# Kernel optimization log

Measured on AMD Instinct MI355X. Metric: run time of the kernel, lower is better.

## Reference

```python
import jax, jax.numpy as jnp
import numpy as np

L, B, D = 1024, 128, 256  # max_seq_len, batch (dialogues), modality feature dim


def _lin_init(key, shape, fan_in):
    s = 1.0 / np.sqrt(fan_in)
    return jax.random.uniform(key, shape, jnp.float32, -s, s)


def setup_inputs() -> dict:
    key = jax.random.key(0)
    ks = jax.random.split(key, 12)
    inp = {
        'a': jax.random.normal(ks[0], (L, B, D), jnp.float32),
        'v': jax.random.normal(ks[1], (L, B, D), jnp.float32),
        'l': jax.random.normal(ks[2], (L, B, D), jnp.float32),
        # all dialogues padded to full length -> fixed node count (jit-friendly)
        'lengths': jnp.full((B,), L, dtype=jnp.int32),
        # modality transforms: Linear(mem_dim, cand_dim)
        'Wa': _lin_init(ks[3], (D, D), D), 'ba': jnp.zeros((D,), jnp.float32),
        'Wv': _lin_init(ks[4], (D, D), D), 'bv': jnp.zeros((D,), jnp.float32),
        'Wl': _lin_init(ks[5], (D, D), D), 'bl': jnp.zeros((D,), jnp.float32),
        # pairwise gates: Linear(3*mem_dim, 1)
        'Wav': _lin_init(ks[6], (1, 3 * D), 3 * D), 'bav': jnp.zeros((1,), jnp.float32),
        'Wal': _lin_init(ks[7], (1, 3 * D), 3 * D), 'bal': jnp.zeros((1,), jnp.float32),
        'Wvl': _lin_init(ks[8], (1, 3 * D), 3 * D), 'bvl': jnp.zeros((1,), jnp.float32),
    }
    return inp


def _graphify(x, lengths):
    # simple_batch_graphify: cat_j x[:lengths[j], j, :].  With lengths == L this is
    # exactly the batch-major flattening of the padded tensor (node order preserved).
    return jnp.transpose(x, (1, 0, 2)).reshape(-1, x.shape[-1])  # (B*L, D)


def reference(a, v, l, lengths, Wa, ba, Wv, bv, Wl, bl, Wav, bav, Wal, bal, Wvl, bvl):
    na = _graphify(a, lengths)  # (N, D)
    nv = _graphify(v, lengths)
    nl = _graphify(l, lengths)

    # MMGatedAttention, att_type='general', modals='avl' (dropout = eval identity)
    ha = jnp.tanh(na @ Wa.T + ba)
    hv = jnp.tanh(nv @ Wv.T + bv)
    hl = jnp.tanh(nl @ Wl.T + bl)

    z_av = jax.nn.sigmoid(jnp.concatenate([na, nv, na * nv], axis=-1) @ Wav.T + bav)  # (N,1)
    h_av = z_av * ha + (1.0 - z_av) * hv

    z_al = jax.nn.sigmoid(jnp.concatenate([na, nl, na * nl], axis=-1) @ Wal.T + bal)
    h_al = z_al * ha + (1.0 - z_al) * hl

    z_vl = jax.nn.sigmoid(jnp.concatenate([nv, nl, nv * nl], axis=-1) @ Wvl.T + bvl)
    h_vl = z_vl * hv + (1.0 - z_vl) * hl

    return jnp.concatenate([h_av, h_al, h_vl], axis=-1)  # (N, 3D)
```

## Files before the change

### kernel.cpp

```cpp
#include <hip/hip_runtime.h>
#include <hip/hip_bf16.h>

#define L_SEQ 1024
#define B_DLG 128
#define D_DIM 256
#define BM 32
#define THREADS 512
#define KSTEPS 8
#define NTILES (L_SEQ / BM)
#define NBLK (B_DLG * NTILES)
#define OBPAD 778

typedef __attribute__((ext_vector_type(8))) short short8;
typedef __attribute__((ext_vector_type(4))) float f32x4;

__device__ __forceinline__ unsigned short f_to_bfbits(float f) {
    unsigned int u = __float_as_uint(f);
    unsigned int r = (u + 0x7FFFu + ((u >> 16) & 1u)) >> 16;
    return (unsigned short)r;
}
__device__ __forceinline__ float fast_tanh(float x) {
    return 1.0f - 2.0f / (__expf(2.0f * x) + 1.0f);
}
__device__ __forceinline__ float fast_sigmoid(float x) {
    return 1.0f / (1.0f + __expf(-x));
}
__device__ __forceinline__ float dot4(float4 x, float4 w) {
    return x.x * w.x + x.y * w.y + x.z * w.z + x.w * w.w;
}

__global__ void wconv_kernel(const float* __restrict__ wa,
                             const float* __restrict__ wv,
                             const float* __restrict__ wl,
                             unsigned short* __restrict__ wb) {
    int i = blockIdx.x * blockDim.x + threadIdx.x;
    int mod  = i >> 13;
    int r    = i & 8191;
    int col  = r >> 5;
    int ks   = (r >> 2) & 7;
    int kblk = r & 3;
    const float* src = (mod == 0) ? wa : (mod == 1) ? wv : wl;
    const float4* s = (const float4*)(src + col * 256 + ks * 32 + kblk * 8);
    float4 lo = s[0], hi = s[1];
    short8 pk;
    pk[0] = (short)f_to_bfbits(lo.x); pk[1] = (short)f_to_bfbits(lo.y);
    pk[2] = (short)f_to_bfbits(lo.z); pk[3] = (short)f_to_bfbits(lo.w);
    pk[4] = (short)f_to_bfbits(hi.x); pk[5] = (short)f_to_bfbits(hi.y);
    pk[6] = (short)f_to_bfbits(hi.z); pk[7] = (short)f_to_bfbits(hi.w);
    int dst = mod * 8192 + (((col >> 4) * 8 + ks) << 6) + kblk * 16 + (col & 15);
    *(short8*)(wb + dst * 8) = pk;
}

__global__ __launch_bounds__(THREADS, 4)
void fused_kernel(const float* __restrict__ a,
                  const float* __restrict__ v,
                  const float* __restrict__ l,
                  const unsigned short* __restrict__ wbf,
                  const float* __restrict__ ba,
                  const float* __restrict__ bv,
                  const float* __restrict__ bl,
                  const float* __restrict__ wav, const float* __restrict__ bav,
                  const float* __restrict__ wal, const float* __restrict__ bal,
                  const float* __restrict__ wvl, const float* __restrict__ bvl,
                  float* __restrict__ out) {
    __shared__ __align__(16) char lds_raw[16 * OBPAD * 4];
    __shared__ float lds_z[3][BM];
#define LDS_A  ((unsigned short (*)[BM][D_DIM])lds_raw)
#define LDS_OB ((float (*)[OBPAD])lds_raw)

    const int tid  = threadIdx.x;
    const int wave = tid >> 6;
    const int lane = tid & 63;
    const int b    = blockIdx.x >> 5;
    const int t0   = (blockIdx.x & (NTILES - 1)) * BM;

    float4 fa[4], fv[4], fl[4];
#pragma unroll
    for (int i = 0; i < BM / 8; ++i) {
        const int row = wave + 8 * i;
        const size_t gbase = ((size_t)(t0 + row) * B_DLG + b) * D_DIM + lane * 4;
        fa[i] = *(const float4*)(a + gbase);
        fv[i] = *(const float4*)(v + gbase);
        fl[i] = *(const float4*)(l + gbase);
    }

    const int k0 = lane * 4;
    float4 gav0 = *(const float4*)(wav + k0);
    float4 gav1 = *(const float4*)(wav + 256 + k0);
    float4 gav2 = *(const float4*)(wav + 512 + k0);
    float4 gal0 = *(const float4*)(wal + k0);
    float4 gal1 = *(const float4*)(wal + 256 + k0);
    float4 gal2 = *(const float4*)(wal + 512 + k0);
    float4 gvl0 = *(const float4*)(wvl + k0);
    float4 gvl1 = *(const float4*)(wvl + 256 + k0);
    float4 gvl2 = *(const float4*)(wvl + 512 + k0);

    {
        const int swz = (wave & 7) << 4;
        const int boff = (lane * 8) ^ swz;
#pragma unroll
        for (int i = 0; i < BM / 8; ++i) {
            const int row = wave + 8 * i;
            ushort4 pa, pv, pl;
            pa.x = f_to_bfbits(fa[i].x); pa.y = f_to_bfbits(fa[i].y);
            pa.z = f_to_bfbits(fa[i].z); pa.w = f_to_bfbits(fa[i].w);
            pv.x = f_to_bfbits(fv[i].x); pv.y = f_to_bfbits(fv[i].y);
            pv.z = f_to_bfbits(fv[i].z); pv.w = f_to_bfbits(fv[i].w);
            pl.x = f_to_bfbits(fl[i].x); pl.y = f_to_bfbits(fl[i].y);
            pl.z = f_to_bfbits(fl[i].z); pl.w = f_to_bfbits(fl[i].w);
            *(ushort4*)((char*)&LDS_A[0][row][0] + boff) = pa;
            *(ushort4*)((char*)&LDS_A[1][row][0] + boff) = pv;
            *(ushort4*)((char*)&LDS_A[2][row][0] + boff) = pl;

            float4 pav, pal, pvl;
            pav.x = fa[i].x * fv[i].x; pav.y = fa[i].y * fv[i].y;
            pav.z = fa[i].z * fv[i].z; pav.w = fa[i].w * fv[i].w;
            pal.x = fa[i].x * fl[i].x; pal.y = fa[i].y * fl[i].y;
            pal.z = fa[i].z * fl[i].z; pal.w = fa[i].w * fl[i].w;
            pvl.x = fv[i].x * fl[i].x; pvl.y = fv[i].y * fl[i].y;
            pvl.z = fv[i].z * fl[i].z; pvl.w = fv[i].w * fl[i].w;
            float s_av = dot4(fa[i], gav0) + dot4(fv[i], gav1) + dot4(pav, gav2);
            float s_al = dot4(fa[i], gal0) + dot4(fl[i], gal1) + dot4(pal, gal2);
            float s_vl = dot4(fv[i], gvl0) + dot4(fl[i], gvl1) + dot4(pvl, gvl2);

#pragma unroll
            for (int off = 1; off < 64; off <<= 1) {
                s_av += __shfl_xor(s_av, off);
                s_al += __shfl_xor(s_al, off);
                s_vl += __shfl_xor(s_vl, off);
            }
            if (lane == 0) {
                lds_z[0][row] = fast_sigmoid(s_av + bav[0]);
                lds_z[1][row] = fast_sigmoid(s_al + bal[0]);
                lds_z[2][row] = fast_sigmoid(s_vl + bvl[0]);
            }
        }
    }
    __syncthreads();

    f32x4 acc[3][2][2];
#pragma unroll
    for (int m = 0; m < 3; ++m)
#pragma unroll
        for (int mt = 0; mt < 2; ++mt)
#pragma unroll
            for (int ct = 0; ct < 2; ++ct)
                acc[m][mt][ct] = (f32x4){0.f, 0.f, 0.f, 0.f};

    const int l15 = lane & 15;
    const int kblk = lane >> 4;
    const int colbase = wave * 32;

#pragma unroll 2
    for (int ks = 0; ks < KSTEPS; ++ks) {
        int kbyte = ks * 64 + kblk * 16;
#pragma unroll
        for (int mod = 0; mod < 3; ++mod) {
            short8 afrag[2];
#pragma unroll
            for (int mt = 0; mt < 2; ++mt) {
                int row = mt * 16 + l15;
                int bo = kbyte ^ ((row & 7) << 4);
                afrag[mt] = *(const short8*)((const char*)&LDS_A[mod][row][0] + bo);
            }
#pragma unroll
            for (int ct = 0; ct < 2; ++ct) {
                const unsigned short* bp = wbf +
                    ((size_t)(((mod * 16 + wave * 2 + ct) * 8 + ks) * 64) + lane) * 8;
                short8 bfrag = *(const short8*)bp;
#pragma unroll
                for (int mt = 0; mt < 2; ++mt)
                    acc[mod][mt][ct] = __builtin_amdgcn_mfma_f32_16x16x32_bf16(
                        afrag[mt], bfrag, acc[mod][mt][ct], 0, 0, 0);
            }
        }
    }

    const int col0 = colbase + l15, col1 = colbase + 16 + l15;
    const float bba0 = ba[col0], bba1 = ba[col1];
    const float bbv0 = bv[col0], bbv1 = bv[col1];
    const float bbl0 = bl[col0], bbl1 = bl[col1];

    const size_t rowbase = (size_t)b * L_SEQ + t0;
#pragma unroll
    for (int half = 0; half < 2; ++half) {
        __syncthreads();
        const int mt = half;
#pragma unroll
        for (int ct = 0; ct < 2; ++ct) {
            const int col = (ct == 0) ? col0 : col1;
            const float bba = (ct == 0) ? bba0 : bba1;
            const float bbv = (ct == 0) ? bbv0 : bbv1;
            const float bbl = (ct == 0) ? bbl0 : bbl1;
#pragma unroll
            for (int r = 0; r < 4; ++r) {
                const int rh = kblk * 4 + r;
                float ta = fast_tanh(acc[0][mt][ct][r] + bba);
                float tv = fast_tanh(acc[1][mt][ct][r] + bbv);
                float tl = fast_tanh(acc[2][mt][ct][r] + bbl);
                float zav = lds_z[0][mt * 16 + rh];
                float zal = lds_z[1][mt * 16 + rh];
                float zvl = lds_z[2][mt * 16 + rh];
                LDS_OB[rh][col]             = zav * ta + (1.f - zav) * tv;
                LDS_OB[rh][D_DIM + col]     = zal * ta + (1.f - zal) * tl;
                LDS_OB[rh][2 * D_DIM + col] = zvl * tv + (1.f - zvl) * tl;
            }
        }
        __syncthreads();
#pragma unroll
        for (int r2 = 0; r2 < 2; ++r2) {
            const int row = wave * 2 + r2;
#pragma unroll
            for (int s = 0; s < 3; ++s) {
                float4 val = *(const float4*)&LDS_OB[row][s * D_DIM + lane * 4];
                *(float4*)(out + (rowbase + half * 16 + row) * (3 * D_DIM)
                               + s * D_DIM + lane * 4) = val;
            }
        }
    }
#undef LDS_A
#undef LDS_OB
}

extern "C" void kernel_launch(void* const* d_in, const int* in_sizes, int n_in,
                              void* d_out, int out_size, void* d_ws, size_t ws_size,
                              hipStream_t stream) {
    const float* a   = (const float*)d_in[0];
    const float* v   = (const float*)d_in[1];
    const float* l   = (const float*)d_in[2];
    const float* Wa  = (const float*)d_in[4];
    const float* ba  = (const float*)d_in[5];
    const float* Wv  = (const float*)d_in[6];
    const float* bv  = (const float*)d_in[7];
    const float* Wl  = (const float*)d_in[8];
    const float* bl  = (const float*)d_in[9];
    const float* Wav = (const float*)d_in[10];
    const float* bav = (const float*)d_in[11];
    const float* Wal = (const float*)d_in[12];
    const float* bal = (const float*)d_in[13];
    const float* Wvl = (const float*)d_in[14];
    const float* bvl = (const float*)d_in[15];
    float* out = (float*)d_out;

    unsigned short* wb = (unsigned short*)d_ws;

    hipLaunchKernelGGL(wconv_kernel, dim3(96), dim3(256), 0, stream, Wa, Wv, Wl, wb);
    hipLaunchKernelGGL(fused_kernel, dim3(NBLK), dim3(THREADS), 0, stream,
                       a, v, l, wb, ba, bv, bl, Wav, bav, Wal, bal, Wvl, bvl, out);
}
```

Baseline: 247.3 us.

## Use per-wave LDS staging for output epilogue to drop block barriers

Replaces the block-wide two-half output staging, which needed __syncthreads between phases, with a per-wave private LDS tile (32x36 floats) that each wave writes and reads back under only a waitcnt. Tanh is now applied once to all accumulators up front, and the gate blend is rewritten as h2 + z*(h1-h2). Output stores become 128-byte row segments per wave instead of full 1 KB rows, which may lower global write coalescing, and the WAR safety against the last MFMA reads relies on the added lds_barrier.

```diff
diff --git a/kernel.cpp b/kernel.cpp
--- a/kernel.cpp
+++ b/kernel.cpp
@@ -9,7 +9,7 @@
 #define KSTEPS 8
 #define NTILES (L_SEQ / BM)
 #define NBLK (B_DLG * NTILES)
-#define OBPAD 778
+#define OBROW 36
 
 typedef __attribute__((ext_vector_type(8))) short short8;
 typedef __attribute__((ext_vector_type(4))) float f32x4;
@@ -27,6 +27,12 @@
 }
 __device__ __forceinline__ float dot4(float4 x, float4 w) {
     return x.x * w.x + x.y * w.y + x.z * w.z + x.w * w.w;
+}
+
+__device__ __forceinline__ void lds_barrier() {
+    asm volatile("s_waitcnt lgkmcnt(0)" ::: "memory");
+    __builtin_amdgcn_s_barrier();
+    __builtin_amdgcn_sched_barrier(0);
 }
 
 __global__ void wconv_kernel(const float* __restrict__ wa,
@@ -63,10 +69,9 @@
                   const float* __restrict__ wal, const float* __restrict__ bal,
                   const float* __restrict__ wvl, const float* __restrict__ bvl,
                   float* __restrict__ out) {
-    __shared__ __align__(16) char lds_raw[16 * OBPAD * 4];
+    __shared__ __align__(16) char lds_raw[3 * BM * D_DIM * 2];
     __shared__ float lds_z[3][BM];
-#define LDS_A  ((unsigned short (*)[BM][D_DIM])lds_raw)
-#define LDS_OB ((float (*)[OBPAD])lds_raw)
+#define LDS_A ((unsigned short (*)[BM][D_DIM])lds_raw)
 
     const int tid  = threadIdx.x;
     const int wave = tid >> 6;
@@ -136,7 +141,7 @@
             }
         }
     }
-    __syncthreads();
+    lds_barrier();
 
     f32x4 acc[3][2][2];
 #pragma unroll
@@ -176,50 +181,55 @@
         }
     }
 
+    lds_barrier();
+
     const int col0 = colbase + l15, col1 = colbase + 16 + l15;
     const float bba0 = ba[col0], bba1 = ba[col1];
     const float bbv0 = bv[col0], bbv1 = bv[col1];
     const float bbl0 = bl[col0], bbl1 = bl[col1];
 
+#pragma unroll
+    for (int mt = 0; mt < 2; ++mt)
+#pragma unroll
+        for (int ct = 0; ct < 2; ++ct)
+#pragma unroll
+            for (int r = 0; r < 4; ++r) {
+                acc[0][mt][ct][r] = fast_tanh(acc[0][mt][ct][r] + (ct ? bba1 : bba0));
+                acc[1][mt][ct][r] = fast_tanh(acc[1][mt][ct][r] + (ct ? bbv1 : bbv0));
+                acc[2][mt][ct][r] = fast_tanh(acc[2][mt][ct][r] + (ct ? bbl1 : bbl0));
+            }
+
+    float* ob = (float*)lds_raw + wave * (BM * OBROW);
     const size_t rowbase = (size_t)b * L_SEQ + t0;
-#pragma unroll
-    for (int half = 0; half < 2; ++half) {
-        __syncthreads();
-        const int mt = half;
-#pragma unroll
-        for (int ct = 0; ct < 2; ++ct) {
-            const int col = (ct == 0) ? col0 : col1;
-            const float bba = (ct == 0) ? bba0 : bba1;
-            const float bbv = (ct == 0) ? bbv0 : bbv1;
-            const float bbl = (ct == 0) ? bbl0 : bbl1;
-#pragma unroll
-            for (int r = 0; r < 4; ++r) {
-                const int rh = kblk * 4 + r;
-                float ta = fast_tanh(acc[0][mt][ct][r] + bba);
-                float tv = fast_tanh(acc[1][mt][ct][r] + bbv);
-                float tl = fast_tanh(acc[2][mt][ct][r] + bbl);
-                float zav = lds_z[0][mt * 16 + rh];
-                float zal = lds_z[1][mt * 16 + rh];
-                float zvl = lds_z[2][mt * 16 + rh];
-                LDS_OB[rh][col]             = zav * ta + (1.f - zav) * tv;
-                LDS_OB[rh][D_DIM + col]     = zal * ta + (1.f - zal) * tl;
-                LDS_OB[rh][2 * D_DIM + col] = zvl * tv + (1.f - zvl) * tl;
-            }
+
+#pragma unroll
+    for (int sec = 0; sec < 3; ++sec) {
+        const int mA = (sec == 2) ? 1 : 0;
+        const int mB = (sec == 0) ? 1 : 2;
+#pragma unroll
+        for (int mt = 0; mt < 2; ++mt)
+#pragma unroll
+            for (int ct = 0; ct < 2; ++ct)
+#pragma unroll
+                for (int r = 0; r < 4; ++r) {
+                    const int row = mt * 16 + kblk * 4 + r;
+                    const float h1 = acc[mA][mt][ct][r];
+                    const float h2 = acc[mB][mt][ct][r];
+                    const float z  = lds_z[sec][row];
+                    ob[row * OBROW + ct * 16 + l15] = h2 + z * (h1 - h2);
+                }
+        asm volatile("s_waitcnt lgkmcnt(0)" ::: "memory");
+        __builtin_amdgcn_sched_barrier(0);
+#pragma unroll
+        for (int q = 0; q < 4; ++q) {
+            const int rt   = q * 8 + (lane >> 3);
+            const int colq = lane & 7;
+            float4 val = *(const float4*)&ob[rt * OBROW + colq * 4];
+            *(float4*)(out + (rowbase + rt) * (3 * D_DIM)
+                           + sec * D_DIM + wave * 32 + colq * 4) = val;
         }
-        __syncthreads();
-#pragma unroll
-        for (int r2 = 0; r2 < 2; ++r2) {
-            const int row = wave * 2 + r2;
-#pragma unroll
-            for (int s = 0; s < 3; ++s) {
-                float4 val = *(const float4*)&LDS_OB[row][s * D_DIM + lane * 4];
-                *(float4*)(out + (rowbase + half * 16 + row) * (3 * D_DIM)
-                               + s * D_DIM + lane * 4) = val;
-            }
-        }
     }
 #undef LDS_A
-#undef LDS_OB
 }
 
 extern "C" void kernel_launch(void* const* d_in, const int* in_sizes, int n_in,
```

Result: slower. 255.4 us (+3.2%).

## Split fused kernel into pack and GEMM kernels via workspace fragments

Applied to the files above, without the earlier changes.

Splits the single fused kernel into two. A pack kernel converts a/v/l to bf16 MFMA-fragment layout and computes the sigmoid gates, writing both to workspace. A GEMM kernel then reads those fragments directly from global memory, applies tanh and the gating, and writes output through a per-wave LDS staging buffer. This separates the gate/conversion phase from the matrix-multiply phase and lowers LDS pressure in the GEMM. The cost is an extra round trip of bf16 fragments and gates through HBM, and an extra launch; the old fused kernel is kept as a fallback when the workspace is too small.

```diff
diff --git a/kernel.cpp b/kernel.cpp
--- a/kernel.cpp
+++ b/kernel.cpp
@@ -8,8 +8,16 @@
 #define THREADS 512
 #define KSTEPS 8
 #define NTILES (L_SEQ / BM)
-#define NBLK (B_DLG * NTILES)
+#define NTILE_TOT (B_DLG * NTILES)
+#define OBROW 36
 #define OBPAD 778
+
+#define WS_WB_BYTES   ((size_t)(3 * 65536 * 2))
+#define WS_AFRAG_OFF  WS_WB_BYTES
+#define WS_AFRAG_BYTES ((size_t)NTILE_TOT * 48 * 1024)
+#define WS_Z_OFF      (WS_AFRAG_OFF + WS_AFRAG_BYTES)
+#define WS_Z_BYTES    ((size_t)3 * L_SEQ * B_DLG * 4)
+#define WS_NEED       (WS_Z_OFF + WS_Z_BYTES)
 
 typedef __attribute__((ext_vector_type(8))) short short8;
 typedef __attribute__((ext_vector_type(4))) float f32x4;
@@ -52,21 +60,16 @@
 }
 
 __global__ __launch_bounds__(THREADS, 4)
-void fused_kernel(const float* __restrict__ a,
-                  const float* __restrict__ v,
-                  const float* __restrict__ l,
-                  const unsigned short* __restrict__ wbf,
-                  const float* __restrict__ ba,
-                  const float* __restrict__ bv,
-                  const float* __restrict__ bl,
-                  const float* __restrict__ wav, const float* __restrict__ bav,
-                  const float* __restrict__ wal, const float* __restrict__ bal,
-                  const float* __restrict__ wvl, const float* __restrict__ bvl,
-                  float* __restrict__ out) {
-    __shared__ __align__(16) char lds_raw[16 * OBPAD * 4];
+void pack_kernel(const float* __restrict__ a,
+                 const float* __restrict__ v,
+                 const float* __restrict__ l,
+                 const float* __restrict__ wav, const float* __restrict__ bav,
+                 const float* __restrict__ wal, const float* __restrict__ bal,
+                 const float* __restrict__ wvl, const float* __restrict__ bvl,
+                 unsigned short* __restrict__ afrag,
+                 float* __restrict__ zbuf) {
+    __shared__ __align__(16) unsigned short lds_a[3][BM][D_DIM];
     __shared__ float lds_z[3][BM];
-#define LDS_A  ((unsigned short (*)[BM][D_DIM])lds_raw)
-#define LDS_OB ((float (*)[OBPAD])lds_raw)
 
     const int tid  = threadIdx.x;
     const int wave = tid >> 6;
@@ -76,7 +79,7 @@
 
     float4 fa[4], fv[4], fl[4];
 #pragma unroll
-    for (int i = 0; i < BM / 8; ++i) {
+    for (int i = 0; i < 4; ++i) {
         const int row = wave + 8 * i;
         const size_t gbase = ((size_t)(t0 + row) * B_DLG + b) * D_DIM + lane * 4;
         fa[i] = *(const float4*)(a + gbase);
@@ -99,7 +102,218 @@
         const int swz = (wave & 7) << 4;
         const int boff = (lane * 8) ^ swz;
 #pragma unroll
-        for (int i = 0; i < BM / 8; ++i) {
+        for (int i = 0; i < 4; ++i) {
+            const int row = wave + 8 * i;
+            ushort4 pa, pv, pl;
+            pa.x = f_to_bfbits(fa[i].x); pa.y = f_to_bfbits(fa[i].y);
+            pa.z = f_to_bfbits(fa[i].z); pa.w = f_to_bfbits(fa[i].w);
+            pv.x = f_to_bfbits(fv[i].x); pv.y = f_to_bfbits(fv[i].y);
+            pv.z = f_to_bfbits(fv[i].z); pv.w = f_to_bfbits(fv[i].w);
+            pl.x = f_to_bfbits(fl[i].x); pl.y = f_to_bfbits(fl[i].y);
+            pl.z = f_to_bfbits(fl[i].z); pl.w = f_to_bfbits(fl[i].w);
+            *(ushort4*)((char*)&lds_a[0][row][0] + boff) = pa;
+            *(ushort4*)((char*)&lds_a[1][row][0] + boff) = pv;
+            *(ushort4*)((char*)&lds_a[2][row][0] + boff) = pl;
+
+            float4 pav, pal, pvl;
+            pav.x = fa[i].x * fv[i].x; pav.y = fa[i].y * fv[i].y;
+            pav.z = fa[i].z * fv[i].z; pav.w = fa[i].w * fv[i].w;
+            pal.x = fa[i].x * fl[i].x; pal.y = fa[i].y * fl[i].y;
+            pal.z = fa[i].z * fl[i].z; pal.w = fa[i].w * fl[i].w;
+            pvl.x = fv[i].x * fl[i].x; pvl.y = fv[i].y * fl[i].y;
+            pvl.z = fv[i].z * fl[i].z; pvl.w = fv[i].w * fl[i].w;
+            float s_av = dot4(fa[i], gav0) + dot4(fv[i], gav1) + dot4(pav, gav2);
+            float s_al = dot4(fa[i], gal0) + dot4(fl[i], gal1) + dot4(pal, gal2);
+            float s_vl = dot4(fv[i], gvl0) + dot4(fl[i], gvl1) + dot4(pvl, gvl2);
+#pragma unroll
+            for (int off = 1; off < 64; off <<= 1) {
+                s_av += __shfl_xor(s_av, off);
+                s_al += __shfl_xor(s_al, off);
+                s_vl += __shfl_xor(s_vl, off);
+            }
+            if (lane == 0) {
+                lds_z[0][row] = fast_sigmoid(s_av + bav[0]);
+                lds_z[1][row] = fast_sigmoid(s_al + bal[0]);
+                lds_z[2][row] = fast_sigmoid(s_vl + bvl[0]);
+            }
+        }
+    }
+    __syncthreads();
+
+    const int l15 = lane & 15;
+    const int kblk = lane >> 4;
+    const size_t tbase = (size_t)blockIdx.x * 48;
+#pragma unroll
+    for (int j = 0; j < 6; ++j) {
+        const int c   = wave * 6 + j;
+        const int mod = c >> 4;
+        const int rem = c & 15;
+        const int mt  = rem >> 3;
+        const int ks  = rem & 7;
+        const int row = mt * 16 + l15;
+        const int bo  = (ks * 64 + kblk * 16) ^ ((row & 7) << 4);
+        short8 frag = *(const short8*)((const char*)&lds_a[mod][row][0] + bo);
+        *(short8*)(afrag + (tbase + c) * 512 + lane * 8) = frag;
+    }
+    if (tid < 96) {
+        const int sec = tid >> 5, row = tid & 31;
+        zbuf[sec * (L_SEQ * B_DLG) + blockIdx.x * BM + row] = lds_z[sec][row];
+    }
+}
+
+__global__ __launch_bounds__(THREADS, 4)
+void gemm_kernel(const unsigned short* __restrict__ afrag,
+                 const unsigned short* __restrict__ wbf,
+                 const float* __restrict__ zbuf,
+                 const float* __restrict__ ba,
+                 const float* __restrict__ bv,
+                 const float* __restrict__ bl,
+                 float* __restrict__ out) {
+    __shared__ __align__(16) float lds_ob[8][BM * OBROW];
+
+    const int tid  = threadIdx.x;
+    const int wave = tid >> 6;
+    const int lane = tid & 63;
+    const int l15  = lane & 15;
+    const int kblk = lane >> 4;
+    const size_t tile = blockIdx.x;
+
+    f32x4 acc[3][2][2];
+#pragma unroll
+    for (int m = 0; m < 3; ++m)
+#pragma unroll
+        for (int mt = 0; mt < 2; ++mt)
+#pragma unroll
+            for (int ct = 0; ct < 2; ++ct)
+                acc[m][mt][ct] = (f32x4){0.f, 0.f, 0.f, 0.f};
+
+#pragma unroll 2
+    for (int ks = 0; ks < KSTEPS; ++ks) {
+#pragma unroll
+        for (int mod = 0; mod < 3; ++mod) {
+            short8 afr[2];
+#pragma unroll
+            for (int mt = 0; mt < 2; ++mt) {
+                const int c = (mod * 2 + mt) * 8 + ks;
+                afr[mt] = *(const short8*)(afrag + (tile * 48 + c) * 512 + lane * 8);
+            }
+#pragma unroll
+            for (int ct = 0; ct < 2; ++ct) {
+                const unsigned short* bp = wbf +
+                    ((size_t)(((mod * 16 + wave * 2 + ct) * 8 + ks) * 64) + lane) * 8;
+                short8 bfrag = *(const short8*)bp;
+#pragma unroll
+                for (int mt = 0; mt < 2; ++mt)
+                    acc[mod][mt][ct] = __builtin_amdgcn_mfma_f32_16x16x32_bf16(
+                        afr[mt], bfrag, acc[mod][mt][ct], 0, 0, 0);
+            }
+        }
+    }
+
+    float zr[3][2][4];
+#pragma unroll
+    for (int sec = 0; sec < 3; ++sec)
+#pragma unroll
+        for (int mt = 0; mt < 2; ++mt)
+#pragma unroll
+            for (int r = 0; r < 4; ++r)
+                zr[sec][mt][r] = zbuf[sec * (L_SEQ * B_DLG) + tile * BM
+                                      + mt * 16 + kblk * 4 + r];
+
+    const int colbase = wave * 32;
+    const int col0 = colbase + l15, col1 = colbase + 16 + l15;
+    const float bba0 = ba[col0], bba1 = ba[col1];
+    const float bbv0 = bv[col0], bbv1 = bv[col1];
+    const float bbl0 = bl[col0], bbl1 = bl[col1];
+#pragma unroll
+    for (int mt = 0; mt < 2; ++mt)
+#pragma unroll
+        for (int ct = 0; ct < 2; ++ct)
+#pragma unroll
+            for (int r = 0; r < 4; ++r) {
+                acc[0][mt][ct][r] = fast_tanh(acc[0][mt][ct][r] + (ct ? bba1 : bba0));
+                acc[1][mt][ct][r] = fast_tanh(acc[1][mt][ct][r] + (ct ? bbv1 : bbv0));
+                acc[2][mt][ct][r] = fast_tanh(acc[2][mt][ct][r] + (ct ? bbl1 : bbl0));
+            }
+
+    float* ob = lds_ob[wave];
+    const size_t rowbase = tile * BM;
+#pragma unroll
+    for (int sec = 0; sec < 3; ++sec) {
+        const int mA = (sec == 2) ? 1 : 0;
+        const int mB = (sec == 0) ? 1 : 2;
+#pragma unroll
+        for (int mt = 0; mt < 2; ++mt)
+#pragma unroll
+            for (int ct = 0; ct < 2; ++ct)
+#pragma unroll
+                for (int r = 0; r < 4; ++r) {
+                    const int row = mt * 16 + kblk * 4 + r;
+                    const float h1 = acc[mA][mt][ct][r];
+                    const float h2 = acc[mB][mt][ct][r];
+                    const float z  = zr[sec][mt][r];
+                    ob[row * OBROW + ct * 16 + l15] = h2 + z * (h1 - h2);
+                }
+        asm volatile("s_waitcnt lgkmcnt(0)" ::: "memory");
+        __builtin_amdgcn_sched_barrier(0);
+#pragma unroll
+        for (int q = 0; q < 4; ++q) {
+            const int rt   = q * 8 + (lane >> 3);
+            const int colq = lane & 7;
+            float4 val = *(const float4*)&ob[rt * OBROW + colq * 4];
+            *(float4*)(out + (rowbase + rt) * (3 * D_DIM)
+                           + sec * D_DIM + wave * 32 + colq * 4) = val;
+        }
+    }
+}
+
+__global__ __launch_bounds__(THREADS, 4)
+void fused_fallback(const float* __restrict__ a,
+                    const float* __restrict__ v,
+                    const float* __restrict__ l,
+                    const unsigned short* __restrict__ wbf,
+                    const float* __restrict__ ba,
+                    const float* __restrict__ bv,
+                    const float* __restrict__ bl,
+                    const float* __restrict__ wav, const float* __restrict__ bav,
+                    const float* __restrict__ wal, const float* __restrict__ bal,
+                    const float* __restrict__ wvl, const float* __restrict__ bvl,
+                    float* __restrict__ out) {
+    __shared__ __align__(16) char lds_raw[16 * OBPAD * 4];
+    __shared__ float lds_z[3][BM];
+#define LDS_A  ((unsigned short (*)[BM][D_DIM])lds_raw)
+#define LDS_OB ((float (*)[OBPAD])lds_raw)
+
+    const int tid  = threadIdx.x;
+    const int wave = tid >> 6;
+    const int lane = tid & 63;
+    const int b    = blockIdx.x >> 5;
+    const int t0   = (blockIdx.x & (NTILES - 1)) * BM;
+
+    float4 fa[4], fv[4], fl[4];
+#pragma unroll
+    for (int i = 0; i < 4; ++i) {
+        const int row = wave + 8 * i;
+        const size_t gbase = ((size_t)(t0 + row) * B_DLG + b) * D_DIM + lane * 4;
+        fa[i] = *(const float4*)(a + gbase);
+        fv[i] = *(const float4*)(v + gbase);
+        fl[i] = *(const float4*)(l + gbase);
+    }
+    const int k0 = lane * 4;
+    float4 gav0 = *(const float4*)(wav + k0);
+    float4 gav1 = *(const float4*)(wav + 256 + k0);
+    float4 gav2 = *(const float4*)(wav + 512 + k0);
+    float4 gal0 = *(const float4*)(wal + k0);
+    float4 gal1 = *(const float4*)(wal + 256 + k0);
+    float4 gal2 = *(const float4*)(wal + 512 + k0);
+    float4 gvl0 = *(const float4*)(wvl + k0);
+    float4 gvl1 = *(const float4*)(wvl + 256 + k0);
+    float4 gvl2 = *(const float4*)(wvl + 512 + k0);
+    {
+        const int swz = (wave & 7) << 4;
+        const int boff = (lane * 8) ^ swz;
+#pragma unroll
+        for (int i = 0; i < 4; ++i) {
             const int row = wave + 8 * i;
             ushort4 pa, pv, pl;
             pa.x = f_to_bfbits(fa[i].x); pa.y = f_to_bfbits(fa[i].y);
@@ -111,7 +325,6 @@
             *(ushort4*)((char*)&LDS_A[0][row][0] + boff) = pa;
             *(ushort4*)((char*)&LDS_A[1][row][0] + boff) = pv;
             *(ushort4*)((char*)&LDS_A[2][row][0] + boff) = pl;
-
             float4 pav, pal, pvl;
             pav.x = fa[i].x * fv[i].x; pav.y = fa[i].y * fv[i].y;
             pav.z = fa[i].z * fv[i].z; pav.w = fa[i].w * fv[i].w;
@@ -122,7 +335,6 @@
             float s_av = dot4(fa[i], gav0) + dot4(fv[i], gav1) + dot4(pav, gav2);
             float s_al = dot4(fa[i], gal0) + dot4(fl[i], gal1) + dot4(pal, gal2);
             float s_vl = dot4(fv[i], gvl0) + dot4(fl[i], gvl1) + dot4(pvl, gvl2);
-
 #pragma unroll
             for (int off = 1; off < 64; off <<= 1) {
                 s_av += __shfl_xor(s_av, off);
@@ -146,11 +358,9 @@
 #pragma unroll
             for (int ct = 0; ct < 2; ++ct)
                 acc[m][mt][ct] = (f32x4){0.f, 0.f, 0.f, 0.f};
-
     const int l15 = lane & 15;
     const int kblk = lane >> 4;
     const int colbase = wave * 32;
-
 #pragma unroll 2
     for (int ks = 0; ks < KSTEPS; ++ks) {
         int kbyte = ks * 64 + kblk * 16;
@@ -175,12 +385,10 @@
             }
         }
     }
-
     const int col0 = colbase + l15, col1 = colbase + 16 + l15;
     const float bba0 = ba[col0], bba1 = ba[col1];
     const float bbv0 = bv[col0], bbv1 = bv[col1];
     const float bbl0 = bl[col0], bbl1 = bl[col1];
-
     const size_t rowbase = (size_t)b * L_SEQ + t0;
 #pragma unroll
     for (int half = 0; half < 2; ++half) {
@@ -243,8 +451,18 @@
     float* out = (float*)d_out;
 
     unsigned short* wb = (unsigned short*)d_ws;
-
     hipLaunchKernelGGL(wconv_kernel, dim3(96), dim3(256), 0, stream, Wa, Wv, Wl, wb);
-    hipLaunchKernelGGL(fused_kernel, dim3(NBLK), dim3(THREADS), 0, stream,
-                       a, v, l, wb, ba, bv, bl, Wav, bav, Wal, bal, Wvl, bvl, out);
-}
+
+    if (ws_size >= WS_NEED) {
+        unsigned short* afrag = (unsigned short*)((char*)d_ws + WS_AFRAG_OFF);
+        float* zbuf = (float*)((char*)d_ws + WS_Z_OFF);
+        hipLaunchKernelGGL(pack_kernel, dim3(NTILE_TOT), dim3(THREADS), 0, stream,
+                           a, v, l, Wav, bav, Wal, bal, Wvl, bvl, afrag, zbuf);
+        hipLaunchKernelGGL(gemm_kernel, dim3(NTILE_TOT), dim3(THREADS), 0, stream,
+                           afrag, wb, zbuf, ba, bv, bl, out);
+    } else {
+        hipLaunchKernelGGL(fused_fallback, dim3(NTILE_TOT), dim3(THREADS), 0, stream,
+                           a, v, l, wb, ba, bv, bl,
+                           Wav, bav, Wal, bal, Wvl, bvl, out);
+    }
+}
```

New measurement: 379.1 us. +53.3%, slower.
